# Kernel tuning notes

Hardware: AMD Instinct MI355X
Metric: run time of the kernel (lower is better)

Reference implementation:

```python
import math
import jax, jax.numpy as jnp
import numpy as np

B, T, C, H = 2, 1024, 1024, 16
D = C // H
NEG = -jnp.inf


def setup_inputs() -> dict:
    key = jax.random.key(0)
    ks = jax.random.split(key, 4)
    x_star = jax.random.normal(ks[0], (B, T, C), jnp.float32)
    x_hat = jax.random.normal(ks[1], (B, T, C), jnp.float32)
    # attn_masks semantics: True = keep. star-keys: causal; hat-keys: diagonal only.
    keep_star = jnp.broadcast_to(jnp.tril(jnp.ones((T, T), bool)), (B, T, T))
    keep_hat = jnp.broadcast_to(jnp.eye(T, dtype=bool), (B, T, T))
    W_attn = jax.random.normal(ks[2], (C, 3 * C), jnp.float32) * (1.0 / math.sqrt(C))
    b_attn = jnp.zeros((3 * C,), jnp.float32)
    W_proj = jax.random.normal(ks[3], (C, C), jnp.float32) * (1.0 / math.sqrt(C))
    b_proj = jnp.zeros((C,), jnp.float32)
    return dict(x_star=x_star, x_hat=x_hat, keep_star=keep_star, keep_hat=keep_hat,
                W_attn=W_attn, b_attn=b_attn, W_proj=W_proj, b_proj=b_proj)


def _interleave(x_star, x_hat, keep_star, keep_hat, W_attn, b_attn, W_proj, b_proj):
    def qkv(x):
        q, k, v = jnp.split(x @ W_attn + b_attn, 3, axis=-1)
        r = lambda t: t.reshape(B, T, H, D).transpose(0, 2, 1, 3)  # (B,H,T,D)
        return r(q), r(k), r(v)

    q_s, k_s, v_s = qkv(x_star)
    q_h, k_h, v_h = qkv(x_hat)

    scale = 1.0 / math.sqrt(D)
    attend = lambda q, k: jnp.einsum('bhqd,bhkd->bhqk', q, k) * scale

    # blocking masks (True = block), broadcast over heads
    mask_star = ~keep_star[:, None, :, :]
    mask_hat = ~keep_hat[:, None, :, :]
    mask_causal = ~jnp.tril(jnp.ones((T, T), bool))[None, None]

    def mlp(y):  # (B,H,T,D) -> (B,T,C)
        y = y.transpose(0, 2, 1, 3).reshape(B, T, C)
        return y @ W_proj + b_proj  # resid_dropout is identity in eval

    # star stream: plain causal self-attention
    att_star = jnp.where(mask_causal, NEG, attend(q_s, k_s))
    y_star = mlp(jax.nn.softmax(att_star, axis=-1) @ v_s)

    # hat stream: merge two score streams (hat queries vs star keys / hat keys)
    att_hs = jnp.where(mask_star, NEG, attend(q_h, k_s))
    att_hh = jnp.where(mask_hat, NEG, attend(q_h, k_h))
    merged = jnp.where(jnp.isinf(att_hh), att_hs, att_hh)
    p = jax.nn.softmax(merged, axis=-1)
    y_hat = (jnp.where(mask_star, 0.0, p) @ v_s
             + jnp.where(mask_hat, 0.0, p) @ v_h)
    y_hat = mlp(y_hat)
    return y_star, y_hat


def reference(x_star, x_hat, keep_star, keep_hat, W_attn, b_attn, W_proj, b_proj):
    return _interleave(x_star, x_hat, keep_star, keep_hat, W_attn, b_attn, W_proj, b_proj)
```

## Files before the change

kernel.cpp:

```cpp
#include <hip/hip_runtime.h>
#include <math.h>

#define T_ 1024
#define C_ 1024
#define H_ 16
#define D_ 64
#define B_ 2
#define M2 (B_*T_*C_)
#define QSC 0.18033688f

typedef __attribute__((ext_vector_type(8))) short bf16x8;
typedef __attribute__((ext_vector_type(8))) unsigned short ushort8;
typedef __attribute__((ext_vector_type(4))) float f32x4;

__device__ inline float fast_exp2(float x) {
  return __builtin_amdgcn_exp2f(x);
}

__device__ inline unsigned short f2bf(float f) {
  unsigned int u = __float_as_uint(f);
  u += 0x7fff + ((u >> 16) & 1);
  return (unsigned short)(u >> 16);
}
__device__ inline float bf2f(unsigned short u) {
  return __uint_as_float(((unsigned int)u) << 16);
}
__device__ inline unsigned int pack2bf(float lo, float hi) {
  unsigned int ul = __float_as_uint(lo);
  unsigned int uh = __float_as_uint(hi);
  ul += 0x7fff + ((ul >> 16) & 1);
  uh += 0x7fff + ((uh >> 16) & 1);
  return (ul >> 16) | (uh & 0xffff0000u);
}

__device__ inline void load16(unsigned short* lds, const unsigned short* g) {
  __builtin_amdgcn_global_load_lds(
      (const __attribute__((address_space(1))) unsigned int*)g,
      (__attribute__((address_space(3))) unsigned int*)lds, 16, 0, 0);
}

__global__ __launch_bounds__(256) void convert_x(
    const float* __restrict__ xs, const float* __restrict__ xh,
    unsigned short* __restrict__ Xbf)
{
  size_t c = (size_t)blockIdx.x * 256 + threadIdx.x;
  size_t e = c * 4;
  const float* src = (e < (size_t)2048 * 1024) ? (xs + e)
                                               : (xh + e - (size_t)2048 * 1024);
  float4 v = *(const float4*)src;
  ushort4 o;
  o.x = f2bf(v.x); o.y = f2bf(v.y); o.z = f2bf(v.z); o.w = f2bf(v.w);
  *(ushort4*)(Xbf + e) = o;
}

__global__ __launch_bounds__(256) void transpose_w(
    const float* __restrict__ Win, unsigned short* __restrict__ Wout, int N)
{
  __shared__ float Ts[64][65];
  const int n0 = blockIdx.x * 64, k0 = blockIdx.y * 64;
  const int tid = threadIdx.x;
#pragma unroll
  for (int p = 0; p < 4; ++p) {
    int chunk = tid + p * 256;
    int r = chunk >> 4, c4 = chunk & 15;
    float4 v = *(const float4*)(Win + (size_t)(k0 + r) * N + n0 + c4 * 4);
    Ts[r][c4*4+0] = v.x; Ts[r][c4*4+1] = v.y;
    Ts[r][c4*4+2] = v.z; Ts[r][c4*4+3] = v.w;
  }
  __syncthreads();
#pragma unroll
  for (int p = 0; p < 2; ++p) {
    int chunk = tid + p * 256;
    int n = chunk >> 3, kq = chunk & 7;
    ushort8 o;
#pragma unroll
    for (int j = 0; j < 8; ++j) o[j] = f2bf(Ts[kq * 8 + j][n]);
    *(ushort8*)(Wout + (size_t)(n0 + n) * 1024 + k0 + kq * 8) = o;
  }
}

#define GEMM_MAIN_LOOP(Aptr, Bptr)                                             \
  for (int k0 = 0; k0 < 1024; k0 += 64) {                                      \
    __syncthreads();                                                           \
    _Pragma("unroll")                                                          \
    for (int it = 0; it < 4; ++it) {                                           \
      int chunk = tid + it * 256;                                              \
      int row = chunk >> 3, cq = chunk & 7;                                    \
      int gq = cq ^ (row & 7);                                                 \
      load16(As + chunk * 8, Aptr + (size_t)(row0 + row) * 1024 + k0 + gq*8);  \
      load16(Bs + chunk * 8, Bptr + (size_t)(col0 + row) * 1024 + k0 + gq*8);  \
    }                                                                          \
    __syncthreads();                                                           \
    _Pragma("unroll")                                                          \
    for (int kb = 0; kb < 2; ++kb) {                                           \
      bf16x8 af[4], bfr[4];                                                    \
      int q = kb * 4 + quad;                                                   \
      _Pragma("unroll")                                                        \
      for (int mt = 0; mt < 4; ++mt) {                                         \
        int m = wm * 64 + mt * 16 + lane16;                                    \
        af[mt] = *(const bf16x8*)&As[m * 64 + (q ^ (m & 7)) * 8];              \
      }                                                                        \
      _Pragma("unroll")                                                        \
      for (int nt = 0; nt < 4; ++nt) {                                         \
        int n = wn * 64 + nt * 16 + lane16;                                    \
        bfr[nt] = *(const bf16x8*)&Bs[n * 64 + (q ^ (n & 7)) * 8];             \
      }                                                                        \
      _Pragma("unroll")                                                        \
      for (int mt = 0; mt < 4; ++mt)                                           \
        _Pragma("unroll")                                                      \
        for (int nt = 0; nt < 4; ++nt)                                         \
          acc[mt][nt] = __builtin_amdgcn_mfma_f32_16x16x32_bf16(               \
              af[mt], bfr[nt], acc[mt][nt], 0, 0, 0);                          \
    }                                                                          \
  }

__global__ __launch_bounds__(256) void qkv_mfma(
    const unsigned short* __restrict__ A,
    const unsigned short* __restrict__ Bt,
    const float* __restrict__ bias,
    unsigned short* __restrict__ qkv)
{
  __shared__ __align__(16) unsigned short As[128 * 64];
  __shared__ __align__(16) unsigned short Bs[128 * 64];
  const int tid = threadIdx.x;
  const int col0 = blockIdx.x * 128;
  const int row0 = blockIdx.y * 128;
  const int w = tid >> 6, lane = tid & 63;
  const int lane16 = lane & 15, quad = lane >> 4;
  const int wm = w >> 1, wn = w & 1;
  f32x4 acc[4][4];
#pragma unroll
  for (int mt = 0; mt < 4; ++mt)
#pragma unroll
    for (int nt = 0; nt < 4; ++nt) acc[mt][nt] = (f32x4){0.f, 0.f, 0.f, 0.f};

  GEMM_MAIN_LOOP(A, Bt)

#pragma unroll
  for (int mt = 0; mt < 4; ++mt) {
#pragma unroll
    for (int nt = 0; nt < 4; ++nt) {
      int gn = col0 + wn * 64 + nt * 16 + lane16;
      int which = gn >> 10, c = gn & 1023;
      int h = c >> 6, d = c & 63;
      float bv = bias[gn];
#pragma unroll
      for (int r = 0; r < 4; ++r) {
        int gm = row0 + wm * 64 + mt * 16 + quad * 4 + r;
        int s = gm >> 11, b = (gm >> 10) & 1, t = gm & 1023;
        float val = acc[mt][nt][r] + bv;
        if (which == 0) val *= QSC;
        size_t idx;
        if (which == 2 && s == 0)
          idx = (size_t)2 * M2 + ((size_t)(b * 16 + h) * 64 + d) * 1024 + t;
        else
          idx = (size_t)(s * 3 + which) * M2 +
                ((size_t)(b * 16 + h) * 1024 + t) * 64 + d;
        qkv[idx] = f2bf(val);
      }
    }
  }
}

__global__ __launch_bounds__(256) void proj_mfma(
    const unsigned short* __restrict__ A,
    const unsigned short* __restrict__ Bt,
    const float* __restrict__ bias,
    float* __restrict__ out)
{
  __shared__ __align__(16) unsigned short As[128 * 64];
  __shared__ __align__(16) unsigned short Bs[128 * 64];
  const int tid = threadIdx.x;
  const int col0 = blockIdx.x * 128;
  const int row0 = blockIdx.y * 128;
  const int w = tid >> 6, lane = tid & 63;
  const int lane16 = lane & 15, quad = lane >> 4;
  const int wm = w >> 1, wn = w & 1;
  f32x4 acc[4][4];
#pragma unroll
  for (int mt = 0; mt < 4; ++mt)
#pragma unroll
    for (int nt = 0; nt < 4; ++nt) acc[mt][nt] = (f32x4){0.f, 0.f, 0.f, 0.f};

  GEMM_MAIN_LOOP(A, Bt)

#pragma unroll
  for (int mt = 0; mt < 4; ++mt) {
#pragma unroll
    for (int nt = 0; nt < 4; ++nt) {
      int gn = col0 + wn * 64 + nt * 16 + lane16;
      float bv = bias[gn];
#pragma unroll
      for (int r = 0; r < 4; ++r) {
        int gm = row0 + wm * 64 + mt * 16 + quad * 4 + r;
        out[(size_t)gm * 1024 + gn] = acc[mt][nt][r] + bv;
      }
    }
  }
}

__global__ __launch_bounds__(256) void attn_kernel(
    const unsigned short* __restrict__ ws, unsigned short* __restrict__ Y)
{
  __shared__ __align__(16) unsigned short Qs[64 * 64];
  __shared__ __align__(16) unsigned short Ks[2][64 * 64];
  __shared__ __align__(16) unsigned short Vts[2][64 * 64];
  __shared__ __align__(16) unsigned short Ps[4][16][72];
  __shared__ float diag[64];

  const int tid = threadIdx.x;
  const int bx  = blockIdx.x;
  const int inner = bx & 63;
  const int h = inner & 15;
  const int b = (inner >> 4) & 1;
  const int s = (inner >> 5) & 1;
  const int qt = 15 - (bx >> 6);
  const int i0 = qt * 64;
  const size_t hb = (size_t)(b * H_ + h) * T_ * D_;

  const unsigned short* Qg  = ws + (size_t)(s ? 3 : 0) * M2 + hb;
  const unsigned short* Kg  = ws + (size_t)1 * M2 + hb;
  const unsigned short* VTg = ws + (size_t)2 * M2 + hb;
  const unsigned short* Khg = ws + (size_t)4 * M2 + hb;
  const unsigned short* Vhg = ws + (size_t)5 * M2 + hb;

  const int lane = tid & 63;
  const int w = tid >> 6;
  const int lane16 = lane & 15, quad = lane >> 4;
  const int wq0 = w * 16;

#pragma unroll
  for (int it = 0; it < 2; ++it) {
    int ch = tid + it * 256;
    int row = ch >> 3, cq = ch & 7, gq = cq ^ (row & 7);
    load16(Qs + ch * 8, Qg + (size_t)(i0 + row) * 64 + gq * 8);
    load16(&Ks[0][ch * 8], Kg + (size_t)(0 * 64 + row) * 64 + gq * 8);
    load16(&Vts[0][ch * 8], VTg + (size_t)row * 1024 + 0 * 64 + gq * 8);
  }
  __syncthreads();

  bf16x8 qf[2];
  {
    int m = wq0 + lane16;
    qf[0] = *(const bf16x8*)&Qs[m * 64 + ((quad) ^ (m & 7)) * 8];
    qf[1] = *(const bf16x8*)&Qs[m * 64 + ((4 + quad) ^ (m & 7)) * 8];
  }
  if (s == 1) {
    if (tid < 64) {
      const unsigned short* kh = Khg + (size_t)(i0 + tid) * 64;
      float sum = 0.f;
#pragma unroll
      for (int c = 0; c < 8; ++c) {
        bf16x8 qv = *(const bf16x8*)&Qs[tid * 64 + (c ^ (tid & 7)) * 8];
        ushort8 kv = *(const ushort8*)(kh + c * 8);
#pragma unroll
        for (int j = 0; j < 8; ++j)
          sum += bf2f((unsigned short)qv[j]) * bf2f(kv[j]);
      }
      diag[tid] = sum;
    }
    __syncthreads();
  }

  float mrun = -INFINITY, lrun = 0.f;
  f32x4 O[4];
#pragma unroll
  for (int nt = 0; nt < 4; ++nt) O[nt] = (f32x4){0.f, 0.f, 0.f, 0.f};

  for (int kt = 0; kt <= qt; ++kt) {
    const int cur = kt & 1;
    if (kt < qt) {
      const int nxt = 1 - cur;
#pragma unroll
      for (int it = 0; it < 2; ++it) {
        int ch = tid + it * 256;
        int row = ch >> 3, cq = ch & 7, gq = cq ^ (row & 7);
        load16(&Ks[nxt][ch * 8], Kg + (size_t)((kt + 1) * 64 + row) * 64 + gq * 8);
        load16(&Vts[nxt][ch * 8], VTg + (size_t)row * 1024 + (kt + 1) * 64 + gq * 8);
      }
    }

    f32x4 St[4];
#pragma unroll
    for (int mt = 0; mt < 4; ++mt) St[mt] = (f32x4){0.f, 0.f, 0.f, 0.f};
#pragma unroll
    for (int kb = 0; kb < 2; ++kb) {
#pragma unroll
      for (int mt = 0; mt < 4; ++mt) {
        int m = mt * 16 + lane16;
        bf16x8 kf = *(const bf16x8*)&Ks[cur][m * 64 + ((kb * 4 + quad) ^ (m & 7)) * 8];
        St[mt] = __builtin_amdgcn_mfma_f32_16x16x32_bf16(kf, qf[kb], St[mt], 0, 0, 0);
      }
    }

    if (kt == qt) {
      const int kstar = wq0 + lane16;
      const float dv = (s == 1) ? diag[kstar] : 0.f;
#pragma unroll
      for (int mt = 0; mt < 4; ++mt)
#pragma unroll
        for (int r = 0; r < 4; ++r) {
          int key = mt * 16 + quad * 4 + r;
          float v = St[mt][r];
          if (s == 1 && key == kstar) v = dv;
          if (key > kstar) v = -INFINITY;
          St[mt][r] = v;
        }
    }

    float mt_ = -INFINITY;
#pragma unroll
    for (int mt = 0; mt < 4; ++mt)
#pragma unroll
      for (int r = 0; r < 4; ++r) mt_ = fmaxf(mt_, St[mt][r]);
    mt_ = fmaxf(mt_, __shfl_xor(mt_, 16, 64));
    mt_ = fmaxf(mt_, __shfl_xor(mt_, 32, 64));
    float mnew = fmaxf(mrun, mt_);
    float alpha = fast_exp2(mrun - mnew);
    mrun = mnew;
    float rsum = 0.f;
#pragma unroll
    for (int mt = 0; mt < 4; ++mt)
#pragma unroll
      for (int r = 0; r < 4; ++r) {
        float p = fast_exp2(St[mt][r] - mnew);
        St[mt][r] = p;
        rsum += p;
      }
    rsum += __shfl_xor(rsum, 16, 64);
    rsum += __shfl_xor(rsum, 32, 64);
    lrun = lrun * alpha + rsum;

#pragma unroll
    for (int mt = 0; mt < 4; ++mt) {
      *(unsigned int*)&Ps[w][lane16][mt * 16 + quad * 4] =
          pack2bf(St[mt][0], St[mt][1]);
      *(unsigned int*)&Ps[w][lane16][mt * 16 + quad * 4 + 2] =
          pack2bf(St[mt][2], St[mt][3]);
    }

    float a4[4];
#pragma unroll
    for (int r = 0; r < 4; ++r) a4[r] = __shfl(alpha, quad * 4 + r, 16);
#pragma unroll
    for (int nt = 0; nt < 4; ++nt)
#pragma unroll
      for (int r = 0; r < 4; ++r) O[nt][r] *= a4[r];

#pragma unroll
    for (int kb = 0; kb < 2; ++kb) {
      bf16x8 pa = *(const bf16x8*)&Ps[w][lane16][kb * 32 + quad * 8];
#pragma unroll
      for (int nt = 0; nt < 4; ++nt) {
        int n = nt * 16 + lane16;
        bf16x8 vb = *(const bf16x8*)&Vts[cur][n * 64 + ((kb * 4 + quad) ^ (n & 7)) * 8];
        O[nt] = __builtin_amdgcn_mfma_f32_16x16x32_bf16(pa, vb, O[nt], 0, 0, 0);
      }
    }

    if (s == 1 && kt == qt) {
      float pd = fast_exp2(diag[wq0 + lane16] - mrun);
      float p4[4];
#pragma unroll
      for (int r = 0; r < 4; ++r) p4[r] = __shfl(pd, quad * 4 + r, 16);
#pragma unroll
      for (int r = 0; r < 4; ++r) {
        const unsigned short* vh = Vhg + (size_t)(i0 + wq0 + quad * 4 + r) * 64;
#pragma unroll
        for (int nt = 0; nt < 4; ++nt)
          O[nt][r] += p4[r] * bf2f(vh[nt * 16 + lane16]);
      }
    }
    __syncthreads();
  }

  float l4[4];
#pragma unroll
  for (int r = 0; r < 4; ++r) l4[r] = __shfl(lrun, quad * 4 + r, 16);
#pragma unroll
  for (int r = 0; r < 4; ++r) {
    int gi = i0 + wq0 + quad * 4 + r;
    float inv = 1.f / l4[r];
    unsigned short* yo = Y + ((size_t)(s * 2048 + b * 1024 + gi)) * 1024 + h * 64;
#pragma unroll
    for (int nt = 0; nt < 4; ++nt)
      yo[nt * 16 + lane16] = f2bf(O[nt][r] * inv);
  }
}

extern "C" void kernel_launch(void* const* d_in, const int* in_sizes, int n_in,
                              void* d_out, int out_size, void* d_ws, size_t ws_size,
                              hipStream_t stream) {
  (void)in_sizes; (void)n_in; (void)out_size; (void)ws_size;
  const float* xs = (const float*)d_in[0];
  const float* xh = (const float*)d_in[1];
  const float* Wa = (const float*)d_in[4];
  const float* ba = (const float*)d_in[5];
  const float* Wp = (const float*)d_in[6];
  const float* bp = (const float*)d_in[7];

  unsigned short* qkv = (unsigned short*)d_ws;
  unsigned short* Ybf = qkv + (size_t)6 * M2;
  unsigned short* Xbf = Ybf + (size_t)4 * 1024 * 1024;
  unsigned short* WaT = Xbf + (size_t)4 * 1024 * 1024;
  unsigned short* WpT = WaT + (size_t)3 * 1024 * 1024;
  float* out = (float*)d_out;

  convert_x  <<<4096, 256, 0, stream>>>(xs, xh, Xbf);
  transpose_w<<<dim3(48, 16), 256, 0, stream>>>(Wa, WaT, 3072);
  transpose_w<<<dim3(16, 16), 256, 0, stream>>>(Wp, WpT, 1024);
  qkv_mfma   <<<dim3(24, 32), 256, 0, stream>>>(Xbf, WaT, ba, qkv);
  attn_kernel<<<dim3(1024), 256, 0, stream>>>(qkv, Ybf);
  proj_mfma  <<<dim3(8, 32), 256, 0, stream>>>(Ybf, WpT, bp, out);
}
```

Baseline: 194.2 us.

## Fuse prep kernels into one launch and retile QKV and projection GEMMs

The x conversion and the two weight transposes are merged into a single prepass launch that branches on block index, removing two kernel launches. The QKV GEMM moves to 512 threads per block with 8 waves, each computing a 64x32 sub-tile, so more waves are resident and per-thread accumulator registers drop. The projection GEMM uses a 128x64 tile, doubling its grid to 512 blocks to fill more compute units. Smaller per-wave tiles lower the MFMA-to-LDS-read ratio, and the fused prepass ties its shared-memory footprint to every block, including the conversion blocks that do not use it.

Result: faster. 181.4 us (-6.6%).

```diff
diff --git a/kernel.cpp b/kernel.cpp
--- a/kernel.cpp
+++ b/kernel.cpp
@@ -39,26 +39,10 @@
       (__attribute__((address_space(3))) unsigned int*)lds, 16, 0, 0);
 }
 
-__global__ __launch_bounds__(256) void convert_x(
-    const float* __restrict__ xs, const float* __restrict__ xh,
-    unsigned short* __restrict__ Xbf)
+__device__ void transpose_tile(const float* __restrict__ Win,
+                               unsigned short* __restrict__ Wout, int N,
+                               int n0, int k0, float (*Ts)[65], int tid)
 {
-  size_t c = (size_t)blockIdx.x * 256 + threadIdx.x;
-  size_t e = c * 4;
-  const float* src = (e < (size_t)2048 * 1024) ? (xs + e)
-                                               : (xh + e - (size_t)2048 * 1024);
-  float4 v = *(const float4*)src;
-  ushort4 o;
-  o.x = f2bf(v.x); o.y = f2bf(v.y); o.z = f2bf(v.z); o.w = f2bf(v.w);
-  *(ushort4*)(Xbf + e) = o;
-}
-
-__global__ __launch_bounds__(256) void transpose_w(
-    const float* __restrict__ Win, unsigned short* __restrict__ Wout, int N)
-{
-  __shared__ float Ts[64][65];
-  const int n0 = blockIdx.x * 64, k0 = blockIdx.y * 64;
-  const int tid = threadIdx.x;
 #pragma unroll
   for (int p = 0; p < 4; ++p) {
     int chunk = tid + p * 256;
@@ -79,42 +63,34 @@
   }
 }
 
-#define GEMM_MAIN_LOOP(Aptr, Bptr)                                             \
-  for (int k0 = 0; k0 < 1024; k0 += 64) {                                      \
-    __syncthreads();                                                           \
-    _Pragma("unroll")                                                          \
-    for (int it = 0; it < 4; ++it) {                                           \
-      int chunk = tid + it * 256;                                              \
-      int row = chunk >> 3, cq = chunk & 7;                                    \
-      int gq = cq ^ (row & 7);                                                 \
-      load16(As + chunk * 8, Aptr + (size_t)(row0 + row) * 1024 + k0 + gq*8);  \
-      load16(Bs + chunk * 8, Bptr + (size_t)(col0 + row) * 1024 + k0 + gq*8);  \
-    }                                                                          \
-    __syncthreads();                                                           \
-    _Pragma("unroll")                                                          \
-    for (int kb = 0; kb < 2; ++kb) {                                           \
-      bf16x8 af[4], bfr[4];                                                    \
-      int q = kb * 4 + quad;                                                   \
-      _Pragma("unroll")                                                        \
-      for (int mt = 0; mt < 4; ++mt) {                                         \
-        int m = wm * 64 + mt * 16 + lane16;                                    \
-        af[mt] = *(const bf16x8*)&As[m * 64 + (q ^ (m & 7)) * 8];              \
-      }                                                                        \
-      _Pragma("unroll")                                                        \
-      for (int nt = 0; nt < 4; ++nt) {                                         \
-        int n = wn * 64 + nt * 16 + lane16;                                    \
-        bfr[nt] = *(const bf16x8*)&Bs[n * 64 + (q ^ (n & 7)) * 8];             \
-      }                                                                        \
-      _Pragma("unroll")                                                        \
-      for (int mt = 0; mt < 4; ++mt)                                           \
-        _Pragma("unroll")                                                      \
-        for (int nt = 0; nt < 4; ++nt)                                         \
-          acc[mt][nt] = __builtin_amdgcn_mfma_f32_16x16x32_bf16(               \
-              af[mt], bfr[nt], acc[mt][nt], 0, 0, 0);                          \
-    }                                                                          \
-  }
-
-__global__ __launch_bounds__(256) void qkv_mfma(
+__global__ __launch_bounds__(256) void prepass(
+    const float* __restrict__ xs, const float* __restrict__ xh,
+    const float* __restrict__ Wa, const float* __restrict__ Wp,
+    unsigned short* __restrict__ Xbf, unsigned short* __restrict__ WaT,
+    unsigned short* __restrict__ WpT)
+{
+  __shared__ float Ts[64][65];
+  const int bid = blockIdx.x;
+  const int tid = threadIdx.x;
+  if (bid < 4096) {
+    size_t c = (size_t)bid * 256 + tid;
+    size_t e = c * 4;
+    const float* src = (e < (size_t)2048 * 1024) ? (xs + e)
+                                                 : (xh + e - (size_t)2048 * 1024);
+    float4 v = *(const float4*)src;
+    ushort4 o;
+    o.x = f2bf(v.x); o.y = f2bf(v.y); o.z = f2bf(v.z); o.w = f2bf(v.w);
+    *(ushort4*)(Xbf + e) = o;
+  } else if (bid < 4864) {
+    int t = bid - 4096;
+    transpose_tile(Wa, WaT, 3072, (t % 48) * 64, (t / 48) * 64, Ts, tid);
+  } else {
+    int t = bid - 4864;
+    transpose_tile(Wp, WpT, 1024, (t % 16) * 64, (t / 16) * 64, Ts, tid);
+  }
+}
+
+__global__ __launch_bounds__(512) void qkv_mfma(
     const unsigned short* __restrict__ A,
     const unsigned short* __restrict__ Bt,
     const float* __restrict__ bias,
@@ -127,20 +103,51 @@
   const int row0 = blockIdx.y * 128;
   const int w = tid >> 6, lane = tid & 63;
   const int lane16 = lane & 15, quad = lane >> 4;
-  const int wm = w >> 1, wn = w & 1;
-  f32x4 acc[4][4];
+  const int wm = w >> 2, wn = w & 3;
+  f32x4 acc[4][2];
 #pragma unroll
   for (int mt = 0; mt < 4; ++mt)
 #pragma unroll
-    for (int nt = 0; nt < 4; ++nt) acc[mt][nt] = (f32x4){0.f, 0.f, 0.f, 0.f};
-
-  GEMM_MAIN_LOOP(A, Bt)
+    for (int nt = 0; nt < 2; ++nt) acc[mt][nt] = (f32x4){0.f, 0.f, 0.f, 0.f};
+
+  for (int k0 = 0; k0 < 1024; k0 += 64) {
+    __syncthreads();
+#pragma unroll
+    for (int it = 0; it < 2; ++it) {
+      int chunk = tid + it * 512;
+      int row = chunk >> 3, cq = chunk & 7, gq = cq ^ (row & 7);
+      load16(As + chunk * 8, A  + (size_t)(row0 + row) * 1024 + k0 + gq * 8);
+      load16(Bs + chunk * 8, Bt + (size_t)(col0 + row) * 1024 + k0 + gq * 8);
+    }
+    __syncthreads();
+#pragma unroll
+    for (int kb = 0; kb < 2; ++kb) {
+      bf16x8 af[4], bfr[2];
+      int q = kb * 4 + quad;
+#pragma unroll
+      for (int mt = 0; mt < 4; ++mt) {
+        int m = wm * 64 + mt * 16 + lane16;
+        af[mt] = *(const bf16x8*)&As[m * 64 + (q ^ (m & 7)) * 8];
+      }
+#pragma unroll
+      for (int nt = 0; nt < 2; ++nt) {
+        int n = wn * 32 + nt * 16 + lane16;
+        bfr[nt] = *(const bf16x8*)&Bs[n * 64 + (q ^ (n & 7)) * 8];
+      }
+#pragma unroll
+      for (int mt = 0; mt < 4; ++mt)
+#pragma unroll
+        for (int nt = 0; nt < 2; ++nt)
+          acc[mt][nt] = __builtin_amdgcn_mfma_f32_16x16x32_bf16(
+              af[mt], bfr[nt], acc[mt][nt], 0, 0, 0);
+    }
+  }
 
 #pragma unroll
   for (int mt = 0; mt < 4; ++mt) {
 #pragma unroll
-    for (int nt = 0; nt < 4; ++nt) {
-      int gn = col0 + wn * 64 + nt * 16 + lane16;
+    for (int nt = 0; nt < 2; ++nt) {
+      int gn = col0 + wn * 32 + nt * 16 + lane16;
       int which = gn >> 10, c = gn & 1023;
       int h = c >> 6, d = c & 63;
       float bv = bias[gn];
@@ -169,26 +176,62 @@
     float* __restrict__ out)
 {
   __shared__ __align__(16) unsigned short As[128 * 64];
-  __shared__ __align__(16) unsigned short Bs[128 * 64];
+  __shared__ __align__(16) unsigned short Bs[64 * 64];
   const int tid = threadIdx.x;
-  const int col0 = blockIdx.x * 128;
+  const int col0 = blockIdx.x * 64;
   const int row0 = blockIdx.y * 128;
   const int w = tid >> 6, lane = tid & 63;
   const int lane16 = lane & 15, quad = lane >> 4;
   const int wm = w >> 1, wn = w & 1;
-  f32x4 acc[4][4];
+  f32x4 acc[4][2];
 #pragma unroll
   for (int mt = 0; mt < 4; ++mt)
 #pragma unroll
-    for (int nt = 0; nt < 4; ++nt) acc[mt][nt] = (f32x4){0.f, 0.f, 0.f, 0.f};
-
-  GEMM_MAIN_LOOP(A, Bt)
+    for (int nt = 0; nt < 2; ++nt) acc[mt][nt] = (f32x4){0.f, 0.f, 0.f, 0.f};
+
+  for (int k0 = 0; k0 < 1024; k0 += 64) {
+    __syncthreads();
+#pragma unroll
+    for (int it = 0; it < 4; ++it) {
+      int chunk = tid + it * 256;
+      int row = chunk >> 3, cq = chunk & 7, gq = cq ^ (row & 7);
+      load16(As + chunk * 8, A + (size_t)(row0 + row) * 1024 + k0 + gq * 8);
+    }
+#pragma unroll
+    for (int it = 0; it < 2; ++it) {
+      int chunk = tid + it * 256;
+      int row = chunk >> 3, cq = chunk & 7, gq = cq ^ (row & 7);
+      load16(Bs + chunk * 8, Bt + (size_t)(col0 + row) * 1024 + k0 + gq * 8);
+    }
+    __syncthreads();
+#pragma unroll
+    for (int kb = 0; kb < 2; ++kb) {
+      bf16x8 af[4], bfr[2];
+      int q = kb * 4 + quad;
+#pragma unroll
+      for (int mt = 0; mt < 4; ++mt) {
+        int m = wm * 64 + mt * 16 + lane16;
+        af[mt] = *(const bf16x8*)&As[m * 64 + (q ^ (m & 7)) * 8];
+      }
+#pragma unroll
+      for (int nt = 0; nt < 2; ++nt) {
+        int n = wn * 32 + nt * 16 + lane16;
+        bfr[nt] = *(const bf16x8*)&Bs[n * 64 + (q ^ (n & 7)) * 8];
+      }
+#pragma unroll
+      for (int mt = 0; mt < 4; ++mt)
+#pragma unroll
+        for (int nt = 0; nt < 2; ++nt)
+          acc[mt][nt] = __builtin_amdgcn_mfma_f32_16x16x32_bf16(
+              af[mt], bfr[nt], acc[mt][nt], 0, 0, 0);
+    }
+  }
 
 #pragma unroll
   for (int mt = 0; mt < 4; ++mt) {
 #pragma unroll
-    for (int nt = 0; nt < 4; ++nt) {
-      int gn = col0 + wn * 64 + nt * 16 + lane16;
+    for (int nt = 0; nt < 2; ++nt) {
+      int gn = col0 + wn * 32 + nt * 16 + lane16;
       float bv = bias[gn];
 #pragma unroll
       for (int r = 0; r < 4; ++r) {
@@ -406,10 +449,8 @@
   unsigned short* WpT = WaT + (size_t)3 * 1024 * 1024;
   float* out = (float*)d_out;
 
-  convert_x  <<<4096, 256, 0, stream>>>(xs, xh, Xbf);
-  transpose_w<<<dim3(48, 16), 256, 0, stream>>>(Wa, WaT, 3072);
-  transpose_w<<<dim3(16, 16), 256, 0, stream>>>(Wp, WpT, 1024);
-  qkv_mfma   <<<dim3(24, 32), 256, 0, stream>>>(Xbf, WaT, ba, qkv);
+  prepass    <<<5120, 256, 0, stream>>>(xs, xh, Wa, Wp, Xbf, WaT, WpT);
+  qkv_mfma   <<<dim3(24, 32), 512, 0, stream>>>(Xbf, WaT, ba, qkv);
   attn_kernel<<<dim3(1024), 256, 0, stream>>>(qkv, Ybf);
-  proj_mfma  <<<dim3(8, 32), 256, 0, stream>>>(Ybf, WpT, bp, out);
-}
+  proj_mfma  <<<dim3(16, 32), 256, 0, stream>>>(Ybf, WpT, bp, out);
+}
```
